# Performance work log

Measured on AMD Instinct MI355X. Metric: run time of the kernel, lower is better.

Reference implementation:

```python
import jax, jax.numpy as jnp
import numpy as np

DIM = 512
B, S = 4, 2048


def _linear_params(key, d_in, d_out):
    kw, kb = jax.random.split(key)
    bound = 1.0 / np.sqrt(d_in)
    W = jax.random.uniform(kw, (d_out, d_in), minval=-bound, maxval=bound, dtype=jnp.float32)
    b = jax.random.uniform(kb, (d_out,), minval=-bound, maxval=bound, dtype=jnp.float32)
    return W, b


def setup_inputs() -> dict:
    key = jax.random.key(0)
    ks = jax.random.split(key, 6)
    x = jax.random.normal(ks[0], (B, S, DIM), dtype=jnp.float32)
    Wq, bq = _linear_params(ks[1], DIM, DIM)
    Wk, bk = _linear_params(ks[2], DIM, DIM)
    Wv, bv = _linear_params(ks[3], DIM, DIM)
    W1, b1 = _linear_params(ks[4], DIM, 4 * DIM)
    W2, b2 = _linear_params(ks[5], 4 * DIM, DIM)
    return {"x": x, "Wq": Wq, "bq": bq, "Wk": Wk, "bk": bk,
            "Wv": Wv, "bv": bv, "W1": W1, "b1": b1, "W2": W2, "b2": b2}


def reference(x, Wq, bq, Wk, bk, Wv, bv, W1, b1, W2, b2):
    # q, k, v projections (torch Linear: x @ W.T + b)
    q = x @ Wq.T + bq          # [B, S, D]
    k = x @ Wk.T + bk
    v = x @ Wv.T + bv
    # unscaled attention, exactly as in the source (no 1/sqrt(d))
    scores = jnp.einsum('bsd,btd->bst', q, k)   # [B, S, S]
    attn = jax.nn.softmax(scores, axis=-1) @ v  # [B, S, D]
    # 2-layer FFN with ReLU
    h = jax.nn.relu(attn @ W1.T + b1)           # [B, S, 4D]
    return h @ W2.T + b2                        # [B, S, D]
```

## Files before the change

kernel.cpp:

```cpp
#include <hip/hip_runtime.h>
#include <hip/hip_bf16.h>

typedef _Float16  f16x8  __attribute__((ext_vector_type(8)));
typedef float     f32x4  __attribute__((ext_vector_type(4)));
typedef unsigned short u16;
typedef u16       u16x4  __attribute__((ext_vector_type(4)));
typedef u16       u16x8  __attribute__((ext_vector_type(8)));

__device__ __forceinline__ u16 f2h_bits(float f) {
    union { _Float16 h; u16 u; } v; v.h = (_Float16)f; return v.u;
}
__device__ __forceinline__ float h2f(u16 b) {
    union { u16 u; _Float16 h; } v; v.u = b; return (float)v.h;
}

__global__ __launch_bounds__(256)
void cvt_all(const float* __restrict__ x,
             const float* __restrict__ Wq, const float* __restrict__ Wk,
             const float* __restrict__ Wv, const float* __restrict__ W1,
             const float* __restrict__ W2, const float* __restrict__ bq,
             const float* __restrict__ bk, const float* __restrict__ bv,
             u16* __restrict__ x16, u16* __restrict__ Wqkv16,
             u16* __restrict__ W116, u16* __restrict__ W216, float* __restrict__ bqkv) {
    const int i = blockIdx.x * 256 + threadIdx.x;
    constexpr int X4 = 8192 * 512 / 4;
    constexpr int S = 512 * 512 / 4, L = 2048 * 512 / 4;
    const float* src; u16* dst; int j;
    if      (i < X4)                 { src = x;  dst = x16;            j = i;                  }
    else if (i < X4 + S)             { src = Wq; dst = Wqkv16;         j = i - X4;             }
    else if (i < X4 + 2 * S)         { src = Wk; dst = Wqkv16 + 4 * S; j = i - X4 - S;         }
    else if (i < X4 + 3 * S)         { src = Wv; dst = Wqkv16 + 8 * S; j = i - X4 - 2 * S;     }
    else if (i < X4 + 3 * S + L)     { src = W1; dst = W116;           j = i - X4 - 3 * S;     }
    else if (i < X4 + 3 * S + 2 * L) { src = W2; dst = W216;           j = i - X4 - 3 * S - L; }
    else if (i < X4 + 3 * S + 2 * L + 384) {
        const int g = (i - X4 - 3 * S - 2 * L) * 4;
#pragma unroll
        for (int t = 0; t < 4; ++t) {
            const int e = g + t;
            bqkv[e] = (e < 512) ? bq[e] : (e < 1024 ? bk[e - 512] : bv[e - 1024]);
        }
        return;
    } else return;
    f32x4 v = ((const f32x4*)src)[j];
    u16x4 h;
#pragma unroll
    for (int t = 0; t < 4; ++t) h[t] = f2h_bits(v[t]);
    ((u16x4*)dst)[j] = h;
}

template<int ROWS>
__device__ __forceinline__ void stage_rows(const u16* __restrict__ g0, int ld, u16* lds, int wl) {
    const int l = threadIdx.x & 63;
    constexpr int CH = ROWS / 64;
#pragma unroll
    for (int i = 0; i < CH; ++i) {
        const int base = (wl * CH + i) << 10;
        const int off  = base + (l << 4);
        const int row  = off >> 6;
        const int cb   = off & 63;
        const u16* g = g0 + (size_t)row * ld + (cb >> 1);
        __builtin_amdgcn_global_load_lds((const __attribute__((address_space(1))) void*)g,
                                         (__attribute__((address_space(3))) void*)((char*)lds + base),
                                         16, 0, 0);
    }
}

template<int BN, int SPLITK, bool RELU, int OMODE, typename TC>
__global__ __launch_bounds__(256 * SPLITK, 4)
void gemm16(const u16* __restrict__ Ag, const u16* __restrict__ Bg,
            const float* __restrict__ bias, TC* __restrict__ C, void* __restrict__ xtra,
            int K, int lda, int ldb, int ldc,
            long sA, long sB, long sC)
{
    const int nx = gridDim.x, ny = gridDim.y;
    const int nwg = nx * ny * gridDim.z;
    int bid = blockIdx.x + nx * (blockIdx.y + ny * blockIdx.z);
    int swz = (bid & 7) * (nwg >> 3) + (bid >> 3);
    const int n0 = (swz % nx) * BN; swz /= nx;
    const int m0 = (swz % ny) * 128;
    const int bz = swz / ny;

    constexpr int FR = (BN == 128) ? 4 : 2;
    constexpr int ATILE = 128 * 32;
    constexpr int BTILE = BN * 32;
    constexpr int BUFSZ = ATILE + BTILE;
    __shared__ __align__(16) u16 smem[SPLITK * 2 * BUFSZ];

    const int l  = threadIdx.x & 63, w = threadIdx.x >> 6;
    const int kw = (SPLITK == 2) ? (w >> 2) : 0;
    const int wl = w & 3;
    const int wr = (BN == 128) ? (wl >> 1) * 64 : wl * 32;
    const int wc = (BN == 128) ? (wl & 1) * 64 : 0;
    const int lr = l & 15, kg = l >> 4;

    const int Kh = K / SPLITK;
    const int kb = kw * Kh;

    const u16* Ab = Ag + (size_t)bz * sA + (size_t)m0 * lda + kb;
    const u16* Bb = Bg + (size_t)bz * sB + (size_t)n0 * ldb + kb;
    C += (size_t)bz * sC;

    u16* mybuf = smem + kw * 2 * BUFSZ;

    auto stage = [&](int buf, int k0) {
        u16* s = mybuf + buf * BUFSZ;
        stage_rows<128>(Ab + k0, lda, s, wl);
        stage_rows<BN>(Bb + k0, ldb, s + ATILE, wl);
    };

    f32x4 acc[FR][4] = {};

    stage(0, 0);
    __syncthreads();
    int cur = 0;
    for (int k0 = 0; k0 < Kh; k0 += 32) {
        if (k0 + 32 < Kh) stage(cur ^ 1, k0 + 32);
        const u16* sA = mybuf + cur * BUFSZ;
        const u16* sB = sA + ATILE;

        f16x8 a[FR], b[4];
#pragma unroll
        for (int i = 0; i < FR; ++i) a[i] = *(const f16x8*)&sA[(wr + i * 16 + lr) * 32 + kg * 8];
#pragma unroll
        for (int i = 0; i < 4; ++i)  b[i] = *(const f16x8*)&sB[(wc + i * 16 + lr) * 32 + kg * 8];
#pragma unroll
        for (int mi = 0; mi < FR; ++mi)
#pragma unroll
            for (int ni = 0; ni < 4; ++ni)
                acc[mi][ni] = __builtin_amdgcn_mfma_f32_16x16x32_f16(a[mi], b[ni], acc[mi][ni], 0, 0, 0);
        __syncthreads();
        cur ^= 1;
    }

    if constexpr (SPLITK == 2) {
        float* red = (float*)smem;
        const int slot = (wl * 64 + l) * (FR * 4);
        if (kw == 1) {
#pragma unroll
            for (int mi = 0; mi < FR; ++mi)
#pragma unroll
                for (int ni = 0; ni < 4; ++ni)
                    *(f32x4*)&red[(slot + mi * 4 + ni) * 4] = acc[mi][ni];
        }
        __syncthreads();
        if (kw == 1) return;
#pragma unroll
        for (int mi = 0; mi < FR; ++mi)
#pragma unroll
            for (int ni = 0; ni < 4; ++ni)
                acc[mi][ni] += *(const f32x4*)&red[(slot + mi * 4 + ni) * 4];
    }

    if constexpr (OMODE == 5) {
        float* MB = (float*)xtra + (size_t)bz * 2048 * 32;
        const int cb = (n0 + wc) >> 6;
#pragma unroll
        for (int mi = 0; mi < FR; ++mi) {
            const int mbase = m0 + wr + mi * 16 + kg * 4;
#pragma unroll
            for (int j = 0; j < 4; ++j) {
                float rmax = fmaxf(fmaxf(acc[mi][0][j], acc[mi][1][j]),
                                   fmaxf(acc[mi][2][j], acc[mi][3][j]));
                rmax = fmaxf(rmax, __shfl_xor(rmax, 1));
                rmax = fmaxf(rmax, __shfl_xor(rmax, 2));
                rmax = fmaxf(rmax, __shfl_xor(rmax, 4));
                rmax = fmaxf(rmax, __shfl_xor(rmax, 8));
                const int row = mbase + j;
                if ((l & 15) == 0) MB[(size_t)row * 32 + cb] = rmax;
#pragma unroll
                for (int ni = 0; ni < 4; ++ni)
                    ((u16*)C)[(size_t)row * ldc + (n0 + wc + ni * 16 + lr)] =
                        f2h_bits(acc[mi][ni][j] - rmax);
            }
        }
        return;
    }

#pragma unroll
    for (int mi = 0; mi < FR; ++mi) {
        const int mbase = m0 + wr + mi * 16 + kg * 4;
#pragma unroll
        for (int ni = 0; ni < 4; ++ni) {
            const int n = n0 + wc + ni * 16 + lr;
            const float bv = bias ? bias[n] : 0.0f;
            if constexpr (OMODE == 4) {
                if (n0 < 1024) {
#pragma unroll
                    for (int j = 0; j < 4; ++j)
                        ((u16*)C)[(size_t)(mbase + j) * ldc + n] = f2h_bits(acc[mi][ni][j] + bv);
                } else {
                    const int d  = n - 1024;
                    const int bb = mbase >> 11;
                    const int s  = mbase & 2047;
                    u16x4 o;
#pragma unroll
                    for (int j = 0; j < 4; ++j) o[j] = f2h_bits(acc[mi][ni][j] + bv);
                    *(u16x4*)((u16*)xtra + ((size_t)bb * 512 + d) * 2048 + s) = o;
                }
            } else {
#pragma unroll
                for (int j = 0; j < 4; ++j) {
                    float x = acc[mi][ni][j] + bv;
                    if constexpr (RELU) x = fmaxf(x, 0.0f);
                    const size_t idx = (size_t)(mbase + j) * ldc + n;
                    if constexpr (OMODE == 0) C[idx] = x;
                    else                      ((u16*)C)[idx] = f2h_bits(x);
                }
            }
        }
    }
}

__global__ __launch_bounds__(256)
void softmax_rows(const u16* __restrict__ S16, const float* __restrict__ MB, u16* __restrict__ P) {
    const int row = blockIdx.x;
    const u16* s = S16 + (size_t)row * 2048;
    u16* p = P + (size_t)row * 2048;
    const int t = threadIdx.x;
    const int l = t & 63, w = t >> 6;
    const float base = MB[(size_t)row * 32 + (t >> 3)];

    u16x8 hv = *(const u16x8*)&s[t * 8];
    float v[8];
#pragma unroll
    for (int j = 0; j < 8; ++j) v[j] = h2f(hv[j]) + base;

    float m = v[0];
#pragma unroll
    for (int j = 1; j < 8; ++j) m = fmaxf(m, v[j]);
#pragma unroll
    for (int off = 1; off < 64; off <<= 1) m = fmaxf(m, __shfl_xor(m, off));

    __shared__ float redm[4], reds[4];
    if (l == 0) redm[w] = m;
    __syncthreads();
    m = fmaxf(fmaxf(redm[0], redm[1]), fmaxf(redm[2], redm[3]));

    float e[8]; float sum = 0.0f;
#pragma unroll
    for (int j = 0; j < 8; ++j) { e[j] = __expf(v[j] - m); sum += e[j]; }
#pragma unroll
    for (int off = 1; off < 64; off <<= 1) sum += __shfl_xor(sum, off);
    if (l == 0) reds[w] = sum;
    __syncthreads();
    sum = reds[0] + reds[1] + reds[2] + reds[3];
    const float inv = 1.0f / sum;

    u16x4 o0, o1;
#pragma unroll
    for (int j = 0; j < 4; ++j) { o0[j] = f2h_bits(e[j] * inv); o1[j] = f2h_bits(e[4 + j] * inv); }
    *(u16x4*)&p[t * 8]     = o0;
    *(u16x4*)&p[t * 8 + 4] = o1;
}

extern "C" void kernel_launch(void* const* d_in, const int* in_sizes, int n_in,
                              void* d_out, int out_size, void* d_ws, size_t ws_size,
                              hipStream_t stream) {
    const float* x  = (const float*)d_in[0];
    const float* Wq = (const float*)d_in[1];
    const float* bq = (const float*)d_in[2];
    const float* Wk = (const float*)d_in[3];
    const float* bk = (const float*)d_in[4];
    const float* Wv = (const float*)d_in[5];
    const float* bv = (const float*)d_in[6];
    const float* W1 = (const float*)d_in[7];
    const float* b1 = (const float*)d_in[8];
    const float* W2 = (const float*)d_in[9];
    const float* b2 = (const float*)d_in[10];
    float* out = (float*)d_out;

    char* ws = (char*)d_ws;
    size_t off = 0;
    auto alloc = [&](size_t bytes) { void* p = ws + off; off += (bytes + 255) & ~(size_t)255; return p; };
    u16* x16    = (u16*)alloc(8192ull * 512 * 2);
    u16* Wqkv16 = (u16*)alloc(1536ull * 512 * 2);
    u16* W116   = (u16*)alloc(2048ull * 512 * 2);
    u16* W216   = (u16*)alloc(512ull * 2048 * 2);
    float* bqkv = (float*)alloc(1536 * 4);
    u16* pbuf   = (u16*)alloc(4ull * 2048 * 2048 * 2);
    u16* s16    = (u16*)alloc(4ull * 2048 * 2048 * 2);
    u16* vt     = (u16*)alloc(4ull * 512 * 2048 * 2);
    float* mb   = (float*)alloc(8192ull * 32 * 4);
    u16* qk   = pbuf;
    u16* P    = pbuf;
    u16* attn = x16;
    u16* h    = s16;
    if (ws_size < off) return;

    dim3 blk(256), blk2(512);

    cvt_all<<<dim3(6914), blk, 0, stream>>>(x, Wq, Wk, Wv, W1, W2, bq, bk, bv,
                                            x16, Wqkv16, W116, W216, bqkv);

    gemm16<64, 1, false, 4, u16><<<dim3(24, 64, 1), blk, 0, stream>>>(
        x16, Wqkv16, bqkv, qk, vt, 512, 512, 512, 1024, 0, 0, 0);
    gemm16<128, 1, false, 5, u16><<<dim3(16, 16, 4), blk, 0, stream>>>(
        qk, qk + 512, nullptr, s16, mb, 512, 1024, 1024, 2048,
        2048L * 1024, 2048L * 1024, 2048L * 2048);
    softmax_rows<<<dim3(8192), blk, 0, stream>>>(s16, mb, P);
    gemm16<64, 2, false, 2, u16><<<dim3(8, 16, 4), blk2, 0, stream>>>(
        P, vt, nullptr, attn, nullptr, 2048, 2048, 2048, 512,
        2048L * 2048, 512L * 2048, 2048L * 512);
    gemm16<128, 1, true, 2, u16><<<dim3(16, 64, 1), blk, 0, stream>>>(
        attn, W116, b1, h, nullptr, 512, 512, 512, 2048, 0, 0, 0);
    gemm16<64, 2, false, 0, float><<<dim3(8, 64, 1), blk2, 0, stream>>>(
        h, W216, b2, out, nullptr, 2048, 2048, 2048, 512, 0, 0, 0);
}
```

Baseline: 186.0 us.

## Fuse softmax normalization into PV GEMM A-tile load with per-block stats

Drops the separate full-row softmax pass over the 4x2048x2048 score matrix. The QK^T epilogue now also writes per-64-column partial exp-sums beside the block max. A tiny stats kernel combines these into per-block log-scale coefficients, and the P@V GEMM reads raw fp16 scores through registers, applying exp2 with the coefficient before staging into LDS. It also fixes all GEMMs to 128-wide N tiles, halving the grid for the split-K GEMMs. The cost is exp work and register-staged loads in the PV GEMM's inner loop instead of async global-to-LDS loads, plus fewer workgroups for the narrow GEMMs.

```diff
diff --git a/kernel.cpp b/kernel.cpp
--- a/kernel.cpp
+++ b/kernel.cpp
@@ -6,6 +6,8 @@
 typedef unsigned short u16;
 typedef u16       u16x4  __attribute__((ext_vector_type(4)));
 typedef u16       u16x8  __attribute__((ext_vector_type(8)));
+
+#define LOG2E 1.44269504f
 
 __device__ __forceinline__ u16 f2h_bits(float f) {
     union { _Float16 h; u16 u; } v; v.h = (_Float16)f; return v.u;
@@ -65,10 +67,11 @@
     }
 }
 
-template<int BN, int SPLITK, bool RELU, int OMODE, typename TC>
+template<int SPLITK, bool RELU, int OMODE, bool AEXP, typename TC>
 __global__ __launch_bounds__(256 * SPLITK, 4)
 void gemm16(const u16* __restrict__ Ag, const u16* __restrict__ Bg,
-            const float* __restrict__ bias, TC* __restrict__ C, void* __restrict__ xtra,
+            const float* __restrict__ bias, TC* __restrict__ C,
+            void* __restrict__ xtra, const void* __restrict__ xtra2,
             int K, int lda, int ldb, int ldc,
             long sA, long sB, long sC)
 {
@@ -76,21 +79,18 @@
     const int nwg = nx * ny * gridDim.z;
     int bid = blockIdx.x + nx * (blockIdx.y + ny * blockIdx.z);
     int swz = (bid & 7) * (nwg >> 3) + (bid >> 3);
-    const int n0 = (swz % nx) * BN; swz /= nx;
+    const int n0 = (swz % nx) * 128; swz /= nx;
     const int m0 = (swz % ny) * 128;
     const int bz = swz / ny;
 
-    constexpr int FR = (BN == 128) ? 4 : 2;
     constexpr int ATILE = 128 * 32;
-    constexpr int BTILE = BN * 32;
-    constexpr int BUFSZ = ATILE + BTILE;
+    constexpr int BUFSZ = 2 * ATILE;
     __shared__ __align__(16) u16 smem[SPLITK * 2 * BUFSZ];
 
     const int l  = threadIdx.x & 63, w = threadIdx.x >> 6;
     const int kw = (SPLITK == 2) ? (w >> 2) : 0;
     const int wl = w & 3;
-    const int wr = (BN == 128) ? (wl >> 1) * 64 : wl * 32;
-    const int wc = (BN == 128) ? (wl & 1) * 64 : 0;
+    const int wr = (wl >> 1) * 64, wc = (wl & 1) * 64;
     const int lr = l & 15, kg = l >> 4;
 
     const int Kh = K / SPLITK;
@@ -98,46 +98,90 @@
 
     const u16* Ab = Ag + (size_t)bz * sA + (size_t)m0 * lda + kb;
     const u16* Bb = Bg + (size_t)bz * sB + (size_t)n0 * ldb + kb;
+    const float* Cb = AEXP ? ((const float*)xtra2 + (size_t)bz * 2048 * 32 + (size_t)m0 * 32)
+                           : nullptr;
     C += (size_t)bz * sC;
 
     u16* mybuf = smem + kw * 2 * BUFSZ;
 
-    auto stage = [&](int buf, int k0) {
+    u16x8 areg0, areg1; float acof0, acof1;
+    auto stage_issue = [&](int buf, int k0) {
         u16* s = mybuf + buf * BUFSZ;
-        stage_rows<128>(Ab + k0, lda, s, wl);
-        stage_rows<BN>(Bb + k0, ldb, s + ATILE, wl);
+        if constexpr (AEXP) {
+            {
+                const int off = ((wl * 2 + 0) << 10) + (l << 4);
+                const int row = off >> 6, col = (off & 63) >> 1;
+                areg0 = *(const u16x8*)&Ab[(size_t)row * lda + k0 + col];
+                acof0 = Cb[row * 32 + ((kb + k0) >> 6)];
+            }
+            {
+                const int off = ((wl * 2 + 1) << 10) + (l << 4);
+                const int row = off >> 6, col = (off & 63) >> 1;
+                areg1 = *(const u16x8*)&Ab[(size_t)row * lda + k0 + col];
+                acof1 = Cb[row * 32 + ((kb + k0) >> 6)];
+            }
+        } else {
+            stage_rows<128>(Ab + k0, lda, s, wl);
+        }
+        stage_rows<128>(Bb + k0, ldb, s + ATILE, wl);
     };
-
-    f32x4 acc[FR][4] = {};
-
-    stage(0, 0);
+    auto stage_finish = [&](int buf) {
+        if constexpr (AEXP) {
+            u16* s = mybuf + buf * BUFSZ;
+            {
+                const int off = ((wl * 2 + 0) << 10) + (l << 4);
+                u16x8 o;
+#pragma unroll
+                for (int j = 0; j < 8; ++j)
+                    o[j] = f2h_bits(exp2f(h2f(areg0[j]) * LOG2E + acof0));
+                *(u16x8*)((char*)s + off) = o;
+            }
+            {
+                const int off = ((wl * 2 + 1) << 10) + (l << 4);
+                u16x8 o;
+#pragma unroll
+                for (int j = 0; j < 8; ++j)
+                    o[j] = f2h_bits(exp2f(h2f(areg1[j]) * LOG2E + acof1));
+                *(u16x8*)((char*)s + off) = o;
+            }
+        }
+    };
+
+    f32x4 acc[4][4] = {};
+    auto compute = [&](int buf) {
+        const u16* sA = mybuf + buf * BUFSZ;
+        const u16* sB = sA + ATILE;
+        f16x8 a[4], b[4];
+#pragma unroll
+        for (int i = 0; i < 4; ++i) a[i] = *(const f16x8*)&sA[(wr + i * 16 + lr) * 32 + kg * 8];
+#pragma unroll
+        for (int i = 0; i < 4; ++i) b[i] = *(const f16x8*)&sB[(wc + i * 16 + lr) * 32 + kg * 8];
+#pragma unroll
+        for (int mi = 0; mi < 4; ++mi)
+#pragma unroll
+            for (int ni = 0; ni < 4; ++ni)
+                acc[mi][ni] = __builtin_amdgcn_mfma_f32_16x16x32_f16(a[mi], b[ni], acc[mi][ni], 0, 0, 0);
+    };
+
+    stage_issue(0, 0);
+    stage_finish(0);
     __syncthreads();
     int cur = 0;
     for (int k0 = 0; k0 < Kh; k0 += 32) {
-        if (k0 + 32 < Kh) stage(cur ^ 1, k0 + 32);
-        const u16* sA = mybuf + cur * BUFSZ;
-        const u16* sB = sA + ATILE;
-
-        f16x8 a[FR], b[4];
-#pragma unroll
-        for (int i = 0; i < FR; ++i) a[i] = *(const f16x8*)&sA[(wr + i * 16 + lr) * 32 + kg * 8];
-#pragma unroll
-        for (int i = 0; i < 4; ++i)  b[i] = *(const f16x8*)&sB[(wc + i * 16 + lr) * 32 + kg * 8];
-#pragma unroll
-        for (int mi = 0; mi < FR; ++mi)
-#pragma unroll
-            for (int ni = 0; ni < 4; ++ni)
-                acc[mi][ni] = __builtin_amdgcn_mfma_f32_16x16x32_f16(a[mi], b[ni], acc[mi][ni], 0, 0, 0);
+        const bool more = (k0 + 32 < Kh);
+        if (more) stage_issue(cur ^ 1, k0 + 32);
+        compute(cur);
+        if (more) stage_finish(cur ^ 1);
         __syncthreads();
         cur ^= 1;
     }
 
     if constexpr (SPLITK == 2) {
         float* red = (float*)smem;
-        const int slot = (wl * 64 + l) * (FR * 4);
+        const int slot = (wl * 64 + l) * 16;
         if (kw == 1) {
 #pragma unroll
-            for (int mi = 0; mi < FR; ++mi)
+            for (int mi = 0; mi < 4; ++mi)
 #pragma unroll
                 for (int ni = 0; ni < 4; ++ni)
                     *(f32x4*)&red[(slot + mi * 4 + ni) * 4] = acc[mi][ni];
@@ -145,7 +189,7 @@
         __syncthreads();
         if (kw == 1) return;
 #pragma unroll
-        for (int mi = 0; mi < FR; ++mi)
+        for (int mi = 0; mi < 4; ++mi)
 #pragma unroll
             for (int ni = 0; ni < 4; ++ni)
                 acc[mi][ni] += *(const f32x4*)&red[(slot + mi * 4 + ni) * 4];
@@ -153,9 +197,11 @@
 
     if constexpr (OMODE == 5) {
         float* MB = (float*)xtra + (size_t)bz * 2048 * 32;
+        float* SB = (float*)const_cast<void*>(xtra2);
+        SB += (size_t)bz * 2048 * 32;
         const int cb = (n0 + wc) >> 6;
 #pragma unroll
-        for (int mi = 0; mi < FR; ++mi) {
+        for (int mi = 0; mi < 4; ++mi) {
             const int mbase = m0 + wr + mi * 16 + kg * 4;
 #pragma unroll
             for (int j = 0; j < 4; ++j) {
@@ -165,8 +211,18 @@
                 rmax = fmaxf(rmax, __shfl_xor(rmax, 2));
                 rmax = fmaxf(rmax, __shfl_xor(rmax, 4));
                 rmax = fmaxf(rmax, __shfl_xor(rmax, 8));
+                float lsum = 0.0f;
+#pragma unroll
+                for (int ni = 0; ni < 4; ++ni) lsum += __expf(acc[mi][ni][j] - rmax);
+                lsum += __shfl_xor(lsum, 1);
+                lsum += __shfl_xor(lsum, 2);
+                lsum += __shfl_xor(lsum, 4);
+                lsum += __shfl_xor(lsum, 8);
                 const int row = mbase + j;
-                if ((l & 15) == 0) MB[(size_t)row * 32 + cb] = rmax;
+                if (lr == 0) {
+                    MB[(size_t)row * 32 + cb] = rmax;
+                    SB[(size_t)row * 32 + cb] = lsum;
+                }
 #pragma unroll
                 for (int ni = 0; ni < 4; ++ni)
                     ((u16*)C)[(size_t)row * ldc + (n0 + wc + ni * 16 + lr)] =
@@ -177,7 +233,7 @@
     }
 
 #pragma unroll
-    for (int mi = 0; mi < FR; ++mi) {
+    for (int mi = 0; mi < 4; ++mi) {
         const int mbase = m0 + wr + mi * 16 + kg * 4;
 #pragma unroll
         for (int ni = 0; ni < 4; ++ni) {
@@ -212,45 +268,33 @@
 }
 
 __global__ __launch_bounds__(256)
-void softmax_rows(const u16* __restrict__ S16, const float* __restrict__ MB, u16* __restrict__ P) {
-    const int row = blockIdx.x;
-    const u16* s = S16 + (size_t)row * 2048;
-    u16* p = P + (size_t)row * 2048;
-    const int t = threadIdx.x;
-    const int l = t & 63, w = t >> 6;
-    const float base = MB[(size_t)row * 32 + (t >> 3)];
-
-    u16x8 hv = *(const u16x8*)&s[t * 8];
-    float v[8];
-#pragma unroll
-    for (int j = 0; j < 8; ++j) v[j] = h2f(hv[j]) + base;
-
-    float m = v[0];
-#pragma unroll
-    for (int j = 1; j < 8; ++j) m = fmaxf(m, v[j]);
-#pragma unroll
-    for (int off = 1; off < 64; off <<= 1) m = fmaxf(m, __shfl_xor(m, off));
-
-    __shared__ float redm[4], reds[4];
-    if (l == 0) redm[w] = m;
-    __syncthreads();
-    m = fmaxf(fmaxf(redm[0], redm[1]), fmaxf(redm[2], redm[3]));
-
-    float e[8]; float sum = 0.0f;
-#pragma unroll
-    for (int j = 0; j < 8; ++j) { e[j] = __expf(v[j] - m); sum += e[j]; }
-#pragma unroll
-    for (int off = 1; off < 64; off <<= 1) sum += __shfl_xor(sum, off);
-    if (l == 0) reds[w] = sum;
-    __syncthreads();
-    sum = reds[0] + reds[1] + reds[2] + reds[3];
-    const float inv = 1.0f / sum;
-
-    u16x4 o0, o1;
-#pragma unroll
-    for (int j = 0; j < 4; ++j) { o0[j] = f2h_bits(e[j] * inv); o1[j] = f2h_bits(e[4 + j] * inv); }
-    *(u16x4*)&p[t * 8]     = o0;
-    *(u16x4*)&p[t * 8 + 4] = o1;
+void softmax_stats(const float* __restrict__ MB, const float* __restrict__ SB,
+                   float* __restrict__ Cc) {
+    const int row = blockIdx.x * 256 + threadIdx.x;
+    const f32x4* mbp = (const f32x4*)(MB + (size_t)row * 32);
+    const f32x4* sbp = (const f32x4*)(SB + (size_t)row * 32);
+    f32x4 mv[8], sv[8];
+#pragma unroll
+    for (int i = 0; i < 8; ++i) { mv[i] = mbp[i]; sv[i] = sbp[i]; }
+    float m = mv[0][0];
+#pragma unroll
+    for (int i = 0; i < 8; ++i)
+#pragma unroll
+        for (int j = 0; j < 4; ++j) m = fmaxf(m, mv[i][j]);
+    float s = 0.0f;
+#pragma unroll
+    for (int i = 0; i < 8; ++i)
+#pragma unroll
+        for (int j = 0; j < 4; ++j) s += sv[i][j] * __expf(mv[i][j] - m);
+    const float lg = __log2f(s);
+    f32x4* cp = (f32x4*)(Cc + (size_t)row * 32);
+#pragma unroll
+    for (int i = 0; i < 8; ++i) {
+        f32x4 o;
+#pragma unroll
+        for (int j = 0; j < 4; ++j) o[j] = (mv[i][j] - m) * LOG2E - lg;
+        cp[i] = o;
+    }
 }
 
 extern "C" void kernel_launch(void* const* d_in, const int* in_sizes, int n_in,
@@ -277,12 +321,12 @@
     u16* W116   = (u16*)alloc(2048ull * 512 * 2);
     u16* W216   = (u16*)alloc(512ull * 2048 * 2);
     float* bqkv = (float*)alloc(1536 * 4);
-    u16* pbuf   = (u16*)alloc(4ull * 2048 * 2048 * 2);
+    u16* qk     = (u16*)alloc(8192ull * 1024 * 2);
     u16* s16    = (u16*)alloc(4ull * 2048 * 2048 * 2);
     u16* vt     = (u16*)alloc(4ull * 512 * 2048 * 2);
     float* mb   = (float*)alloc(8192ull * 32 * 4);
-    u16* qk   = pbuf;
-    u16* P    = pbuf;
+    float* sb   = (float*)alloc(8192ull * 32 * 4);
+    float* cf   = (float*)alloc(8192ull * 32 * 4);
     u16* attn = x16;
     u16* h    = s16;
     if (ws_size < off) return;
@@ -292,17 +336,17 @@
     cvt_all<<<dim3(6914), blk, 0, stream>>>(x, Wq, Wk, Wv, W1, W2, bq, bk, bv,
                                             x16, Wqkv16, W116, W216, bqkv);
 
-    gemm16<64, 1, false, 4, u16><<<dim3(24, 64, 1), blk, 0, stream>>>(
-        x16, Wqkv16, bqkv, qk, vt, 512, 512, 512, 1024, 0, 0, 0);
-    gemm16<128, 1, false, 5, u16><<<dim3(16, 16, 4), blk, 0, stream>>>(
-        qk, qk + 512, nullptr, s16, mb, 512, 1024, 1024, 2048,
+    gemm16<1, false, 4, false, u16><<<dim3(12, 64, 1), blk, 0, stream>>>(
+        x16, Wqkv16, bqkv, qk, vt, nullptr, 512, 512, 512, 1024, 0, 0, 0);
+    gemm16<1, false, 5, false, u16><<<dim3(16, 16, 4), blk, 0, stream>>>(
+        qk, qk + 512, nullptr, s16, mb, sb, 512, 1024, 1024, 2048,
         2048L * 1024, 2048L * 1024, 2048L * 2048);
-    softmax_rows<<<dim3(8192), blk, 0, stream>>>(s16, mb, P);
-    gemm16<64, 2, false, 2, u16><<<dim3(8, 16, 4), blk2, 0, stream>>>(
-        P, vt, nullptr, attn, nullptr, 2048, 2048, 2048, 512,
+    softmax_stats<<<dim3(32), blk, 0, stream>>>(mb, sb, cf);
+    gemm16<2, false, 2, true, u16><<<dim3(4, 16, 4), blk2, 0, stream>>>(
+        s16, vt, nullptr, attn, nullptr, cf, 2048, 2048, 2048, 512,
         2048L * 2048, 512L * 2048, 2048L * 512);
-    gemm16<128, 1, true, 2, u16><<<dim3(16, 64, 1), blk, 0, stream>>>(
-        attn, W116, b1, h, nullptr, 512, 512, 512, 2048, 0, 0, 0);
-    gemm16<64, 2, false, 0, float><<<dim3(8, 64, 1), blk2, 0, stream>>>(
-        h, W216, b2, out, nullptr, 2048, 2048, 2048, 512, 0, 0, 0);
-}
+    gemm16<1, true, 2, false, u16><<<dim3(16, 64, 1), blk, 0, stream>>>(
+        attn, W116, b1, h, nullptr, nullptr, 512, 512, 512, 2048, 0, 0, 0);
+    gemm16<2, false, 0, false, float><<<dim3(4, 64, 1), blk2, 0, stream>>>(
+        h, W216, b2, out, nullptr, nullptr, 2048, 2048, 2048, 512, 0, 0, 0);
+}
```

Measured after the change: 193.3 us. +4.0%, slower.
